# Kernel optimization log

Measured on AMD Instinct MI355X. Metric: run time of the kernel, lower is better.

## Reference

```python
import jax, jax.numpy as jnp
import numpy as np

D = 1024           # input_size
D2 = 2 * D         # hidden width of the three inner linears
OUT = 1024         # output_size
S = 8192           # tokens per example


def setup_inputs() -> dict:
    key = jax.random.key(0)
    ks = jax.random.split(key, 11)
    def lin(k, fan_in, fan_out):
        bound = 1.0 / np.sqrt(fan_in)
        kw, kb = jax.random.split(k)
        W = jax.random.uniform(kw, (fan_in, fan_out), jnp.float32, -bound, bound)
        b = jax.random.uniform(kb, (fan_out,), jnp.float32, -bound, bound)
        return W, b
    W_in, b_in = lin(ks[0], D, D2)      # reading_example_input
    W_out, b_out = lin(ks[1], D, D2)    # reading_example_output
    W_cat, b_cat = lin(ks[2], D2, D2)   # concatenated_layer_map
    W_fin, b_fin = lin(ks[3], D2, OUT)  # final_map
    return {
        "input_embedding": jax.random.normal(ks[4], (1, S, D), jnp.float32),
        "output_embedding": jax.random.normal(ks[5], (1, S, D), jnp.float32),
        "random_augmentation": jax.random.normal(ks[6], (1, S, D), jnp.float32),
        "W_in": W_in, "b_in": b_in,
        "W_out": W_out, "b_out": b_out,
        "W_cat": W_cat, "b_cat": b_cat,
        "W_fin": W_fin, "b_fin": b_fin,
    }


def reference(input_embedding, output_embedding, random_augmentation,
              W_in, b_in, W_out, b_out, W_cat, b_cat, W_fin, b_fin):
    def march(x, y):
        # x, y: [1, S, D]
        iq = jax.nn.softmax(x @ W_in + b_in, axis=-1)[0]    # [S, 2D]
        oq = jax.nn.softmax(y @ W_out + b_out, axis=-1)[0]  # [S, 2D]
        cat = jnp.concatenate((x, y), axis=-1)[0]           # [S, 2D]
        icm = jax.nn.softmax(cat @ W_cat + b_cat, axis=-1)  # [S, 2D]
        iqk = iq.T @ icm                                    # [2D, 2D]
        oqk = oq.T @ icm                                    # [2D, 2D]
        meta = jax.nn.relu(iqk @ oqk.T)                     # [2D, 2D]
        scale = jnp.sqrt(jnp.float32(icm.shape[-1]))
        res = (icm @ meta) / scale                          # [S, 2D]
        return jax.nn.relu(res @ W_fin + b_fin)             # [S, OUT]

    transformation = march(input_embedding, output_embedding)
    random_desc = march(input_embedding, random_augmentation)
    return (transformation, random_desc)
```

## Files before the change

kernel.cpp:

```cpp
#include <hip/hip_runtime.h>

#define S_TOK 8192
#define DIM   1024
#define DIM2  2048
#define OUTN  1024

typedef __bf16 bf16x8 __attribute__((ext_vector_type(8)));
typedef float  f32x4  __attribute__((ext_vector_type(4)));
typedef short  s16x8  __attribute__((ext_vector_type(8)));
typedef unsigned short u16x4 __attribute__((ext_vector_type(4)));

__device__ __forceinline__ unsigned short f2bf(float x) {
  unsigned u = __builtin_bit_cast(unsigned, x);
  u = (u + 0x7FFFu + ((u >> 16) & 1u)) >> 16;
  return (unsigned short)u;
}
__device__ __forceinline__ float bf2f(unsigned short u) {
  return __builtin_bit_cast(float, (unsigned)u << 16);
}

__device__ __forceinline__ void gld_lds16(const void* g, void* l) {
  auto* g1 = reinterpret_cast<__attribute__((address_space(1))) unsigned*>(
      (unsigned long long)g);
  auto* l3 = reinterpret_cast<__attribute__((address_space(3))) unsigned*>(
      (unsigned long long)l);
  __builtin_amdgcn_global_load_lds(g1, l3, 16, 0, 0);
}

__device__ __forceinline__ int lds_off(int idx, int k) {
  int b = (idx << 7) + (k << 1);
  b ^= ((idx ^ (idx >> 3)) & 7) << 4;
  return b;
}

__global__ __launch_bounds__(256) void cvt_f32_bf16(const float* __restrict__ in,
                                                    unsigned short* __restrict__ out, int n4) {
  int i = blockIdx.x * 256 + threadIdx.x;
  if (i >= n4) return;
  float4 v = ((const float4*)in)[i];
  u16x4 o;
  o[0] = f2bf(v.x); o[1] = f2bf(v.y); o[2] = f2bf(v.z); o[3] = f2bf(v.w);
  *(u16x4*)(out + (size_t)i * 4) = o;
}

template <int F32IN>
__global__ __launch_bounds__(256) void transpose_to_bf16(const void* __restrict__ in,
                                                         unsigned short* __restrict__ out,
                                                         int R, int C) {
  __shared__ unsigned short t[64 * 64];
  const int r0 = blockIdx.y << 6, c0 = blockIdx.x << 6;
  const int tid = threadIdx.x;
#pragma unroll
  for (int i = 0; i < 2; ++i) {
    int ch = tid + (i << 8);
    int r = ch >> 3, c8 = (ch & 7) << 3;
    s16x8 w;
    if (F32IN) {
      const float* p = (const float*)in + (size_t)(r0 + r) * C + c0 + c8;
      float4 a = *(const float4*)p, b = *(const float4*)(p + 4);
      w[0] = (short)f2bf(a.x); w[1] = (short)f2bf(a.y);
      w[2] = (short)f2bf(a.z); w[3] = (short)f2bf(a.w);
      w[4] = (short)f2bf(b.x); w[5] = (short)f2bf(b.y);
      w[6] = (short)f2bf(b.z); w[7] = (short)f2bf(b.w);
    } else {
      w = *(const s16x8*)((const unsigned short*)in + (size_t)(r0 + r) * C + c0 + c8);
    }
    int sw = ((r ^ (r >> 3)) & 7) << 3;
    *(s16x8*)&t[(r << 6) + (c8 ^ sw)] = w;
  }
  __syncthreads();
#pragma unroll
  for (int i = 0; i < 2; ++i) {
    int ch = tid + (i << 8);
    int c = ch >> 3, r8 = (ch & 7) << 3;
    s16x8 w;
#pragma unroll
    for (int j = 0; j < 8; ++j) {
      int rr = r8 + j;
      w[j] = (short)t[(rr << 6) + (c ^ (((rr ^ (rr >> 3)) & 7) << 3))];
    }
    *(s16x8*)(out + (size_t)(c0 + c) * R + r0 + r8) = w;
  }
}

struct SmTab { unsigned short* T[6]; };
__global__ __launch_bounds__(512) void softmax_cols(SmTab tab) {
  unsigned short* T = tab.T[blockIdx.y];
  const int tid = threadIdx.x;
  const int colg = tid & 63, seg = tid >> 6;
  const size_t c = ((size_t)blockIdx.x << 6) + colg;
  float m = -1e30f, s = 0.f;
  for (int n = seg; n < DIM2; n += 8) {
    float v = bf2f(T[(size_t)n * S_TOK + c]);
    float mn = fmaxf(m, v);
    s = s * __expf(m - mn) + __expf(v - mn);
    m = mn;
  }
  __shared__ float redm[512], reds[512];
  redm[tid] = m; reds[tid] = s;
  __syncthreads();
  if (seg == 0) {
    float M = m, S = s;
#pragma unroll
    for (int k = 1; k < 8; ++k) {
      float mk = redm[colg + (k << 6)], sk = reds[colg + (k << 6)];
      float mn = fmaxf(M, mk);
      S = S * __expf(M - mn) + sk * __expf(mk - mn);
      M = mn;
    }
    redm[colg] = M; reds[colg] = 1.0f / S;
  }
  __syncthreads();
  m = redm[colg];
  const float inv = reds[colg];
  for (int n = seg; n < DIM2; n += 8) {
    size_t idx = (size_t)n * S_TOK + c;
    T[idx] = f2bf(__expf(bf2f(T[idx]) - m) * inv);
  }
}

struct GPtr {
  const unsigned short* A[3];
  const unsigned short* Arow2[3];
  const unsigned short* B[3];
  const unsigned short* Bk2[3];
  const float* bias[3];
  void* C[3];
};

template <int ASPLIT, int BSPLIT, int BIAS_ROW, int OUT_BF16>
__global__ __launch_bounds__(256, 3) void gemm_nt(GPtr p, int lda, int ldb, int ldc,
                                                  int K, float scale, int do_relu) {
  __shared__ char lds[32768];
  char* As = lds;
  char* Bs = lds + 16384;
  const int z = blockIdx.z;
  const int tid  = threadIdx.x;
  const int lane = tid & 63;
  const int wave = tid >> 6;
  const int wm = (wave >> 1) << 6;
  const int wn = (wave & 1) << 6;
  const int m0 = blockIdx.y << 7;
  const int n0 = blockIdx.x << 7;

  const unsigned short* Au = p.A[z];
  int mb = m0;
  if (ASPLIT && m0 >= 2048) { Au = p.Arow2[z]; mb = m0 - 2048; }
  const unsigned short* B  = p.B[z];
  const unsigned short* B2 = BSPLIT ? p.Bk2[z] : B;
  const float* bias = p.bias[z];
  void* Cv = p.C[z];

  int srow[4], sgk[4];
#pragma unroll
  for (int i = 0; i < 4; ++i) {
    int c = (wave << 8) + (i << 6) + lane;
    int row = c >> 3, kc = c & 7;
    srow[i] = row;
    sgk[i]  = (kc ^ ((row ^ (row >> 3)) & 7)) << 3;
  }

  f32x4 acc[4][4];
#pragma unroll
  for (int i = 0; i < 4; ++i)
#pragma unroll
    for (int j = 0; j < 4; ++j) acc[i][j] = {0.f, 0.f, 0.f, 0.f};

  for (int k0 = 0; k0 < K; k0 += 64) {
    const unsigned short* bsrc = B;
    int kb = k0;
    if (BSPLIT && k0 >= DIM) { bsrc = B2; kb = k0 - DIM; }
#pragma unroll
    for (int i = 0; i < 4; ++i) {
      char* dA = As + (((wave << 2) + i) << 10);
      char* dB = Bs + (((wave << 2) + i) << 10);
      gld_lds16(Au   + (size_t)(mb + srow[i]) * lda + k0 + sgk[i], dA);
      gld_lds16(bsrc + (size_t)(n0 + srow[i]) * ldb + kb + sgk[i], dB);
    }
    __syncthreads();
#pragma unroll
    for (int ks = 0; ks < 2; ++ks) {
      bf16x8 af[4], bfr[4];
      int kk = (ks << 5) + ((lane >> 4) << 3);
#pragma unroll
      for (int t = 0; t < 4; ++t) {
        af[t]  = *(const bf16x8*)(As + lds_off(wm + (t << 4) + (lane & 15), kk));
        bfr[t] = *(const bf16x8*)(Bs + lds_off(wn + (t << 4) + (lane & 15), kk));
      }
#pragma unroll
      for (int mt = 0; mt < 4; ++mt)
#pragma unroll
        for (int nt = 0; nt < 4; ++nt)
          acc[mt][nt] = __builtin_amdgcn_mfma_f32_16x16x32_bf16(af[mt], bfr[nt], acc[mt][nt], 0, 0, 0);
    }
    __syncthreads();
  }

#pragma unroll
  for (int nt = 0; nt < 4; ++nt) {
    int col = n0 + wn + (nt << 4) + (lane & 15);
    float bcol = (!BIAS_ROW && bias) ? bias[col] : 0.0f;
#pragma unroll
    for (int mt = 0; mt < 4; ++mt) {
      f32x4 a = acc[mt][nt];
#pragma unroll
      for (int r = 0; r < 4; ++r) {
        int rowg = m0 + wm + (mt << 4) + ((lane >> 4) << 2) + r;
        float bv = BIAS_ROW ? (bias ? bias[rowg] : 0.0f) : bcol;
        float v = a[r] * scale + bv;
        if (do_relu) v = fmaxf(v, 0.0f);
        if (OUT_BF16) ((unsigned short*)Cv)[(size_t)rowg * ldc + col] = f2bf(v);
        else          ((float*)Cv)[(size_t)rowg * ldc + col] = v;
      }
    }
  }
}

template <int ASPLIT, int BSPLIT, int BIAS_ROW, int OUT_BF16>
__global__ __launch_bounds__(512, 2) void gemm256(GPtr p, int lda, int ldb, int ldc,
                                                  int K, float scale, int do_relu) {
  __shared__ char lds[131072];
  const int z = blockIdx.z;
  const int tid  = threadIdx.x;
  const int lane = tid & 63;
  const int wave = tid >> 6;
  const int wm   = wave >> 2;
  const int wn   = wave & 3;

  const int gx = gridDim.x;
  const int nwg = gx * gridDim.y;
  int id = blockIdx.y * gx + blockIdx.x;
  id = (id & 7) * (nwg >> 3) + (id >> 3);
  const int n0 = (id % gx) << 8;
  const int m0 = (id / gx) << 8;

  const unsigned short* Au = p.A[z];
  int mb = m0;
  if (ASPLIT && m0 >= 2048) { Au = p.Arow2[z]; mb = m0 - 2048; }
  const unsigned short* Bp = p.B[z];
  const unsigned short* B2 = BSPLIT ? p.Bk2[z] : Bp;
  const float* bias = p.bias[z];
  void* Cv = p.C[z];

  int srow[4], sgk[4];
#pragma unroll
  for (int i = 0; i < 4; ++i) {
    int c = (i << 9) + tid;
    int row = c >> 3, kc = c & 7;
    srow[i] = row;
    sgk[i]  = (kc ^ ((row ^ (row >> 3)) & 7)) << 3;
  }

  auto stage = [&](int t) {
    const int k0 = t << 6;
    char* Abase = lds + ((t & 1) << 16);
    char* Bbase = Abase + 32768;
    const unsigned short* bsrc = Bp;
    int kb = k0;
    if (BSPLIT && k0 >= DIM) { bsrc = B2; kb = k0 - DIM; }
#pragma unroll
    for (int i = 0; i < 4; ++i) {
      gld_lds16(Au   + (size_t)(mb + srow[i]) * lda + k0 + sgk[i],
                Abase + (i << 13) + (wave << 10));
      gld_lds16(bsrc + (size_t)(n0 + srow[i]) * ldb + kb + sgk[i],
                Bbase + (i << 13) + (wave << 10));
    }
  };

  f32x4 acc[8][4];
#pragma unroll
  for (int i = 0; i < 8; ++i)
#pragma unroll
    for (int j = 0; j < 4; ++j) acc[i][j] = {0.f, 0.f, 0.f, 0.f};

  const int NT = K >> 6;
  stage(0);
  stage(1);

  for (int t = 0; t < NT; ++t) {
    if (t + 1 < NT) asm volatile("s_waitcnt vmcnt(8)" ::: "memory");
    else            asm volatile("s_waitcnt vmcnt(0)" ::: "memory");
    __builtin_amdgcn_s_barrier();
    __builtin_amdgcn_sched_barrier(0);
    const char* Ab = lds + ((t & 1) << 16);
    const char* Bb = Ab + 32768;
#pragma unroll
    for (int half = 0; half < 2; ++half) {
      const int kk = (half << 5) + ((lane >> 4) << 3);
      bf16x8 aq[4], bq[4];
#pragma unroll
      for (int nf = 0; nf < 4; ++nf)
        bq[nf] = *(const bf16x8*)(Bb + lds_off((wn << 6) + (nf << 4) + (lane & 15), kk));
#pragma unroll
      for (int mf = 0; mf < 4; ++mf)
        aq[mf] = *(const bf16x8*)(Ab + lds_off((wm << 7) + (mf << 4) + (lane & 15), kk));
      __builtin_amdgcn_s_setprio(1);
#pragma unroll
      for (int mf = 0; mf < 4; ++mf)
#pragma unroll
        for (int nf = 0; nf < 4; ++nf)
          acc[mf][nf] = __builtin_amdgcn_mfma_f32_16x16x32_bf16(aq[mf], bq[nf], acc[mf][nf], 0, 0, 0);
      __builtin_amdgcn_s_setprio(0);
      __builtin_amdgcn_sched_barrier(0);
#pragma unroll
      for (int mf = 0; mf < 4; ++mf)
        aq[mf] = *(const bf16x8*)(Ab + lds_off((wm << 7) + ((mf + 4) << 4) + (lane & 15), kk));
      __builtin_amdgcn_s_setprio(1);
#pragma unroll
      for (int mf = 0; mf < 4; ++mf)
#pragma unroll
        for (int nf = 0; nf < 4; ++nf)
          acc[mf + 4][nf] = __builtin_amdgcn_mfma_f32_16x16x32_bf16(aq[mf], bq[nf], acc[mf + 4][nf], 0, 0, 0);
      __builtin_amdgcn_s_setprio(0);
      __builtin_amdgcn_sched_barrier(0);
    }
    __builtin_amdgcn_s_barrier();
    __builtin_amdgcn_sched_barrier(0);
    if (t + 2 < NT) stage(t + 2);
  }

#pragma unroll
  for (int nf = 0; nf < 4; ++nf) {
    int col = n0 + (wn << 6) + (nf << 4) + (lane & 15);
    float bcol = (!BIAS_ROW && bias) ? bias[col] : 0.0f;
#pragma unroll
    for (int mf = 0; mf < 8; ++mf) {
      f32x4 a = acc[mf][nf];
#pragma unroll
      for (int r = 0; r < 4; ++r) {
        int rowg = m0 + (wm << 7) + (mf << 4) + ((lane >> 4) << 2) + r;
        float bv = BIAS_ROW ? (bias ? bias[rowg] : 0.0f) : bcol;
        float v = a[r] * scale + bv;
        if (do_relu) v = fmaxf(v, 0.0f);
        if (OUT_BF16) ((unsigned short*)Cv)[(size_t)rowg * ldc + col] = f2bf(v);
        else          ((float*)Cv)[(size_t)rowg * ldc + col] = v;
      }
    }
  }
}

extern "C" void kernel_launch(void* const* d_in, const int* in_sizes, int n_in,
                              void* d_out, int out_size, void* d_ws, size_t ws_size,
                              hipStream_t stream) {
  const float* X   = (const float*)d_in[0];
  const float* Y   = (const float*)d_in[1];
  const float* R   = (const float*)d_in[2];
  const float* Wi  = (const float*)d_in[3];
  const float* bi  = (const float*)d_in[4];
  const float* Wo  = (const float*)d_in[5];
  const float* bo  = (const float*)d_in[6];
  const float* Wc  = (const float*)d_in[7];
  const float* bc  = (const float*)d_in[8];
  const float* Wf  = (const float*)d_in[9];
  const float* bf_ = (const float*)d_in[10];
  float* out = (float*)d_out;

  char* ws = (char*)d_ws;
  size_t off = 0;
  auto alloc = [&](size_t b) { char* p = ws + off; off += (b + 255) & ~(size_t)255; return p; };
  unsigned short* Xb   = (unsigned short*)alloc((size_t)S_TOK * DIM  * 2);
  unsigned short* Yb   = (unsigned short*)alloc((size_t)S_TOK * DIM  * 2);
  unsigned short* Rb   = (unsigned short*)alloc((size_t)S_TOK * DIM  * 2);
  unsigned short* WiT  = (unsigned short*)alloc((size_t)DIM2 * DIM  * 2);
  unsigned short* WoT  = (unsigned short*)alloc((size_t)DIM2 * DIM  * 2);
  unsigned short* WcT  = (unsigned short*)alloc((size_t)DIM2 * DIM2 * 2);
  unsigned short* WfT  = (unsigned short*)alloc((size_t)OUTN * DIM2 * 2);
  unsigned short* iqT  = (unsigned short*)alloc((size_t)DIM2 * S_TOK * 2);
  unsigned short* oqT0 = (unsigned short*)alloc((size_t)DIM2 * S_TOK * 2);
  unsigned short* oqT1 = (unsigned short*)alloc((size_t)DIM2 * S_TOK * 2);
  unsigned short* icmT0= (unsigned short*)alloc((size_t)DIM2 * S_TOK * 2);
  unsigned short* icmT1= (unsigned short*)alloc((size_t)DIM2 * S_TOK * 2);
  unsigned short* iqk0 = Xb;
  unsigned short* oqk0 = Xb + (size_t)DIM2*DIM2;
  unsigned short* iqk1 = Yb;
  unsigned short* oqk1 = Yb + (size_t)DIM2*DIM2;
  unsigned short* meta0= iqT;
  unsigned short* meta1= iqT + (size_t)DIM2*DIM2;
  unsigned short* MWT0 = iqT + (size_t)2*DIM2*DIM2;
  unsigned short* MWT1 = iqT + (size_t)2*DIM2*DIM2 + (size_t)OUTN*DIM2;
  unsigned short* icm0 = oqT0;
  unsigned short* icm1 = oqT1;

  auto cvt = [&](const float* s, unsigned short* d, int n) {
    int n4 = n >> 2;
    cvt_f32_bf16<<<dim3((n4 + 255) / 256), dim3(256), 0, stream>>>(s, d, n4);
  };
  cvt(X, Xb, S_TOK * DIM);
  cvt(Y, Yb, S_TOK * DIM);
  cvt(R, Rb, S_TOK * DIM);
  transpose_to_bf16<1><<<dim3(DIM2 / 64, DIM  / 64), 256, 0, stream>>>(Wi, WiT, DIM,  DIM2);
  transpose_to_bf16<1><<<dim3(DIM2 / 64, DIM  / 64), 256, 0, stream>>>(Wo, WoT, DIM,  DIM2);
  transpose_to_bf16<1><<<dim3(DIM2 / 64, DIM2 / 64), 256, 0, stream>>>(Wc, WcT, DIM2, DIM2);
  transpose_to_bf16<1><<<dim3(OUTN / 64, DIM2 / 64), 256, 0, stream>>>(Wf, WfT, DIM2, OUTN);

  const float rscale = 0.022097086912079608f;

  {
    GPtr g{};
    g.A[0] = WiT; g.A[1] = WoT; g.A[2] = WoT;
    g.B[0] = Xb;  g.B[1] = Yb;  g.B[2] = Rb;
    g.bias[0] = bi; g.bias[1] = bo; g.bias[2] = bo;
    g.C[0] = iqT; g.C[1] = oqT0; g.C[2] = oqT1;
    gemm256<0,0,1,1><<<dim3(S_TOK/256, DIM2/256, 3), 512, 0, stream>>>(
        g, DIM, DIM, S_TOK, DIM, 1.f, 0);
  }
  {
    GPtr g{};
    g.A[0] = WcT; g.A[1] = WcT;
    g.B[0] = Xb;  g.B[1] = Xb;
    g.Bk2[0] = Yb; g.Bk2[1] = Rb;
    g.bias[0] = bc; g.bias[1] = bc;
    g.C[0] = icmT0; g.C[1] = icmT1;
    gemm256<0,1,1,1><<<dim3(S_TOK/256, DIM2/256, 2), 512, 0, stream>>>(
        g, DIM2, DIM, S_TOK, DIM2, 1.f, 0);
  }
  {
    SmTab st{};
    st.T[0] = iqT; st.T[1] = oqT0; st.T[2] = oqT1; st.T[3] = icmT0; st.T[4] = icmT1;
    softmax_cols<<<dim3(S_TOK / 64, 5), dim3(512), 0, stream>>>(st);
  }
  {
    GPtr g{};
    g.A[0] = iqT; g.A[1] = iqT;
    g.Arow2[0] = oqT0; g.Arow2[1] = oqT1;
    g.B[0] = icmT0; g.B[1] = icmT1;
    g.C[0] = iqk0; g.C[1] = iqk1;
    gemm256<1,0,0,1><<<dim3(DIM2/256, 4096/256, 2), 512, 0, stream>>>(
        g, S_TOK, S_TOK, DIM2, S_TOK, 1.f, 0);
  }
  transpose_to_bf16<0><<<dim3(S_TOK / 64, DIM2 / 64), 256, 0, stream>>>(icmT0, icm0, DIM2, S_TOK);
  transpose_to_bf16<0><<<dim3(S_TOK / 64, DIM2 / 64), 256, 0, stream>>>(icmT1, icm1, DIM2, S_TOK);
  {
    GPtr g{};
    g.A[0] = iqk0; g.A[1] = iqk1;
    g.B[0] = oqk0; g.B[1] = oqk1;
    g.C[0] = meta0; g.C[1] = meta1;
    gemm_nt<0,0,0,1><<<dim3(DIM2/128, DIM2/128, 2), 256, 0, stream>>>(
        g, DIM2, DIM2, DIM2, DIM2, 1.f, 1);
  }
  {
    GPtr g{};
    g.A[0] = WfT; g.A[1] = WfT;
    g.B[0] = meta0; g.B[1] = meta1;
    g.C[0] = MWT0; g.C[1] = MWT1;
    gemm_nt<0,0,0,1><<<dim3(DIM2/128, OUTN/128, 2), 256, 0, stream>>>(
        g, DIM2, DIM2, DIM2, DIM2, rscale, 0);
  }
  {
    GPtr g{};
    g.A[0] = icm0; g.A[1] = icm1;
    g.B[0] = MWT0; g.B[1] = MWT1;
    g.bias[0] = bf_; g.bias[1] = bf_;
    g.C[0] = out; g.C[1] = out + (size_t)S_TOK * OUTN;
    gemm256<0,0,0,0><<<dim3(OUTN/256, S_TOK/256, 2), 512, 0, stream>>>(
        g, DIM2, DIM2, OUTN, DIM2, 1.f, 1);
  }
  (void)in_sizes; (void)n_in; (void)out_size; (void)ws_size;
}
```

Before: 967.7 us.

## Split GEMM256 staging into K-half units interleaved with MFMA phases

Reworks the 256x256 GEMM main loop so each 64-wide K tile is staged as four separate units (A/B for each 32-wide K half). The loads for the next tile are issued between the four MFMA phases of the current tile, replacing the previous two-tile-ahead prefetch. The LDS layout changes to per-half 64-byte rows with a new XOR swizzle, and explicit lgkmcnt waits plus extra barriers are added. The aim is to spread global-to-LDS traffic evenly across compute. The cost is more barriers per iteration and a shorter prefetch distance, which could expose load latency.

```diff
diff --git a/kernel.cpp b/kernel.cpp
--- a/kernel.cpp
+++ b/kernel.cpp
@@ -131,7 +131,7 @@
 template <int ASPLIT, int BSPLIT, int BIAS_ROW, int OUT_BF16>
 __global__ __launch_bounds__(256, 3) void gemm_nt(GPtr p, int lda, int ldb, int ldc,
                                                   int K, float scale, int do_relu) {
-  __shared__ char lds[32768];
+  __shared__ __align__(16) char lds[32768];
   char* As = lds;
   char* Bs = lds + 16384;
   const int z = blockIdx.z;
@@ -219,7 +219,7 @@
 template <int ASPLIT, int BSPLIT, int BIAS_ROW, int OUT_BF16>
 __global__ __launch_bounds__(512, 2) void gemm256(GPtr p, int lda, int ldb, int ldc,
                                                   int K, float scale, int do_relu) {
-  __shared__ char lds[131072];
+  __shared__ __align__(16) char lds[131072];
   const int z = blockIdx.z;
   const int tid  = threadIdx.x;
   const int lane = tid & 63;
@@ -242,81 +242,129 @@
   const float* bias = p.bias[z];
   void* Cv = p.C[z];
 
-  int srow[4], sgk[4];
-#pragma unroll
-  for (int i = 0; i < 4; ++i) {
-    int c = (i << 9) + tid;
-    int row = c >> 3, kc = c & 7;
-    srow[i] = row;
-    sgk[i]  = (kc ^ ((row ^ (row >> 3)) & 7)) << 3;
-  }
-
-  auto stage = [&](int t) {
+  const int NT = K >> 6;
+
+  int srow_[2], skel_[2];
+#pragma unroll
+  for (int i = 0; i < 2; ++i) {
+    int row = (i << 7) + (wave << 4) + (lane >> 2);
+    srow_[i] = row;
+    skel_[i] = ((lane & 3) ^ ((row >> 1) & 3)) << 3;
+  }
+
+  auto stage_unit = [&](int t, int u) {
     const int k0 = t << 6;
-    char* Abase = lds + ((t & 1) << 16);
-    char* Bbase = Abase + 32768;
-    const unsigned short* bsrc = Bp;
-    int kb = k0;
-    if (BSPLIT && k0 >= DIM) { bsrc = B2; kb = k0 - DIM; }
-#pragma unroll
-    for (int i = 0; i < 4; ++i) {
-      gld_lds16(Au   + (size_t)(mb + srow[i]) * lda + k0 + sgk[i],
-                Abase + (i << 13) + (wave << 10));
-      gld_lds16(bsrc + (size_t)(n0 + srow[i]) * ldb + kb + sgk[i],
-                Bbase + (i << 13) + (wave << 10));
+    const int h  = u >> 1;
+    char* base = lds + ((t & 1) << 16) + ((u & 1) << 15) + (h << 14) + (wave << 10);
+    if (u & 1) {
+      const unsigned short* bsrc = Bp;
+      int kb = k0;
+      if (BSPLIT && k0 >= DIM) { bsrc = B2; kb = k0 - DIM; }
+#pragma unroll
+      for (int i = 0; i < 2; ++i)
+        gld_lds16(bsrc + (size_t)(n0 + srow_[i]) * ldb + kb + (h << 5) + skel_[i],
+                  base + (i << 13));
+    } else {
+#pragma unroll
+      for (int i = 0; i < 2; ++i)
+        gld_lds16(Au + (size_t)(mb + srow_[i]) * lda + k0 + (h << 5) + skel_[i],
+                  base + (i << 13));
     }
   };
 
+  auto rdA = [&](const char* buf, int h, int mf) -> bf16x8 {
+    int row = (wm << 7) + (mf << 4) + (lane & 15);
+    int col = (lane >> 4) ^ ((row >> 1) & 3);
+    return *(const bf16x8*)(buf + (h << 14) + (row << 6) + (col << 4));
+  };
+  auto rdB = [&](const char* buf, int h, int nf) -> bf16x8 {
+    int row = (wn << 6) + (nf << 4) + (lane & 15);
+    int col = (lane >> 4) ^ ((row >> 1) & 3);
+    return *(const bf16x8*)(buf + 32768 + (h << 14) + (row << 6) + (col << 4));
+  };
+
   f32x4 acc[8][4];
 #pragma unroll
   for (int i = 0; i < 8; ++i)
 #pragma unroll
     for (int j = 0; j < 4; ++j) acc[i][j] = {0.f, 0.f, 0.f, 0.f};
 
-  const int NT = K >> 6;
-  stage(0);
-  stage(1);
+  stage_unit(0, 0); stage_unit(0, 1); stage_unit(0, 2); stage_unit(0, 3);
 
   for (int t = 0; t < NT; ++t) {
-    if (t + 1 < NT) asm volatile("s_waitcnt vmcnt(8)" ::: "memory");
-    else            asm volatile("s_waitcnt vmcnt(0)" ::: "memory");
+    const char* buf = lds + ((t & 1) << 16);
+    const bool more = (t + 1 < NT);
+    bf16x8 aq[4], bq[4];
+
+    if (more) { stage_unit(t + 1, 0); asm volatile("s_waitcnt vmcnt(6)" ::: "memory"); }
+    else      { asm volatile("s_waitcnt vmcnt(4)" ::: "memory"); }
     __builtin_amdgcn_s_barrier();
     __builtin_amdgcn_sched_barrier(0);
-    const char* Ab = lds + ((t & 1) << 16);
-    const char* Bb = Ab + 32768;
-#pragma unroll
-    for (int half = 0; half < 2; ++half) {
-      const int kk = (half << 5) + ((lane >> 4) << 3);
-      bf16x8 aq[4], bq[4];
+#pragma unroll
+    for (int nf = 0; nf < 4; ++nf) bq[nf] = rdB(buf, 0, nf);
+#pragma unroll
+    for (int mf = 0; mf < 4; ++mf) aq[mf] = rdA(buf, 0, mf);
+    asm volatile("s_waitcnt lgkmcnt(0)" ::: "memory");
+    __builtin_amdgcn_sched_barrier(0);
+    __builtin_amdgcn_s_setprio(1);
+#pragma unroll
+    for (int mf = 0; mf < 4; ++mf)
 #pragma unroll
       for (int nf = 0; nf < 4; ++nf)
-        bq[nf] = *(const bf16x8*)(Bb + lds_off((wn << 6) + (nf << 4) + (lane & 15), kk));
-#pragma unroll
-      for (int mf = 0; mf < 4; ++mf)
-        aq[mf] = *(const bf16x8*)(Ab + lds_off((wm << 7) + (mf << 4) + (lane & 15), kk));
-      __builtin_amdgcn_s_setprio(1);
-#pragma unroll
-      for (int mf = 0; mf < 4; ++mf)
-#pragma unroll
-        for (int nf = 0; nf < 4; ++nf)
-          acc[mf][nf] = __builtin_amdgcn_mfma_f32_16x16x32_bf16(aq[mf], bq[nf], acc[mf][nf], 0, 0, 0);
-      __builtin_amdgcn_s_setprio(0);
-      __builtin_amdgcn_sched_barrier(0);
-#pragma unroll
-      for (int mf = 0; mf < 4; ++mf)
-        aq[mf] = *(const bf16x8*)(Ab + lds_off((wm << 7) + ((mf + 4) << 4) + (lane & 15), kk));
-      __builtin_amdgcn_s_setprio(1);
-#pragma unroll
-      for (int mf = 0; mf < 4; ++mf)
-#pragma unroll
-        for (int nf = 0; nf < 4; ++nf)
-          acc[mf + 4][nf] = __builtin_amdgcn_mfma_f32_16x16x32_bf16(aq[mf], bq[nf], acc[mf + 4][nf], 0, 0, 0);
-      __builtin_amdgcn_s_setprio(0);
-      __builtin_amdgcn_sched_barrier(0);
-    }
+        acc[mf][nf] = __builtin_amdgcn_mfma_f32_16x16x32_bf16(aq[mf], bq[nf], acc[mf][nf], 0, 0, 0);
+    __builtin_amdgcn_s_setprio(0);
+    __builtin_amdgcn_sched_barrier(0);
     __builtin_amdgcn_s_barrier();
-    __builtin_amdgcn_sched_barrier(0);
-    if (t + 2 < NT) stage(t + 2);
+
+#pragma unroll
+    for (int mf = 0; mf < 4; ++mf) aq[mf] = rdA(buf, 0, mf + 4);
+    if (more) stage_unit(t + 1, 1);
+    asm volatile("s_waitcnt lgkmcnt(0)" ::: "memory");
+    __builtin_amdgcn_sched_barrier(0);
+    __builtin_amdgcn_s_setprio(1);
+#pragma unroll
+    for (int mf = 0; mf < 4; ++mf)
+#pragma unroll
+      for (int nf = 0; nf < 4; ++nf)
+        acc[mf + 4][nf] = __builtin_amdgcn_mfma_f32_16x16x32_bf16(aq[mf], bq[nf], acc[mf + 4][nf], 0, 0, 0);
+    __builtin_amdgcn_s_setprio(0);
+    __builtin_amdgcn_sched_barrier(0);
+    __builtin_amdgcn_s_barrier();
+
+    if (more) { stage_unit(t + 1, 2); asm volatile("s_waitcnt vmcnt(6)" ::: "memory"); }
+    else      { asm volatile("s_waitcnt vmcnt(0)" ::: "memory"); }
+    __builtin_amdgcn_s_barrier();
+    __builtin_amdgcn_sched_barrier(0);
+#pragma unroll
+    for (int nf = 0; nf < 4; ++nf) bq[nf] = rdB(buf, 1, nf);
+#pragma unroll
+    for (int mf = 0; mf < 4; ++mf) aq[mf] = rdA(buf, 1, mf);
+    asm volatile("s_waitcnt lgkmcnt(0)" ::: "memory");
+    __builtin_amdgcn_sched_barrier(0);
+    __builtin_amdgcn_s_setprio(1);
+#pragma unroll
+    for (int mf = 0; mf < 4; ++mf)
+#pragma unroll
+      for (int nf = 0; nf < 4; ++nf)
+        acc[mf][nf] = __builtin_amdgcn_mfma_f32_16x16x32_bf16(aq[mf], bq[nf], acc[mf][nf], 0, 0, 0);
+    __builtin_amdgcn_s_setprio(0);
+    __builtin_amdgcn_sched_barrier(0);
+    __builtin_amdgcn_s_barrier();
+
+#pragma unroll
+    for (int mf = 0; mf < 4; ++mf) aq[mf] = rdA(buf, 1, mf + 4);
+    if (more) stage_unit(t + 1, 3);
+    asm volatile("s_waitcnt lgkmcnt(0)" ::: "memory");
+    __builtin_amdgcn_sched_barrier(0);
+    __builtin_amdgcn_s_setprio(1);
+#pragma unroll
+    for (int mf = 0; mf < 4; ++mf)
+#pragma unroll
+      for (int nf = 0; nf < 4; ++nf)
+        acc[mf + 4][nf] = __builtin_amdgcn_mfma_f32_16x16x32_bf16(aq[mf], bq[nf], acc[mf + 4][nf], 0, 0, 0);
+    __builtin_amdgcn_s_setprio(0);
+    __builtin_amdgcn_sched_barrier(0);
+    __builtin_amdgcn_s_barrier();
   }
 
 #pragma unroll
```

Result: faster. 928.9 us (-4.0%).
